# Performance work log

Hardware: AMD Instinct MI355X
Metric: run time of the kernel (lower is better)

Reference implementation:

```python
import jax, jax.numpy as jnp
import numpy as np

WS = 8            # window_size
N = WS * WS       # tokens per window = 64
C = 512           # dim
TEMB = 512        # temb_dim
H = 8             # num_heads
D = C // H        # head_dim = 64
B = 2048          # number of windows (batch * windows per image)


def _rel_pos_index(ws: int) -> np.ndarray:
    coords = np.stack(np.meshgrid(np.arange(ws), np.arange(ws), indexing='ij'))  # (2, ws, ws)
    flat = coords.reshape(2, -1)                      # (2, N)
    rel = flat[:, :, None] - flat[:, None, :]         # (2, N, N)
    rel = rel.transpose(1, 2, 0).copy()               # (N, N, 2)
    rel[:, :, 0] += ws - 1
    rel[:, :, 1] += ws - 1
    rel[:, :, 0] *= 2 * ws - 1
    return rel.sum(-1)                                # (N, N) int

_RP_INDEX = jnp.asarray(_rel_pos_index(WS))           # (N, N)


def setup_inputs() -> dict:
    key = jax.random.key(0)
    ks = jax.random.split(key, 8)
    std = 0.02
    return {
        'x': jax.random.normal(ks[0], (B, N, C), dtype=jnp.float32),
        'temb': jax.random.normal(ks[1], (B, TEMB), dtype=jnp.float32),
        'w_qkv': jax.random.normal(ks[2], (C, 3 * C), dtype=jnp.float32) * std,
        'b_qkv': jnp.zeros((3 * C,), dtype=jnp.float32),
        'w_qkv_t': jax.random.normal(ks[3], (TEMB, 3 * C), dtype=jnp.float32) * std,
        'w_proj': jax.random.normal(ks[4], (C, C), dtype=jnp.float32) * std,
        'b_proj': jnp.zeros((C,), dtype=jnp.float32),
        'rpb_table': jax.random.normal(ks[5], ((2 * WS - 1) ** 2, H), dtype=jnp.float32) * std,
    }


def reference(x, temb, w_qkv, b_qkv, w_qkv_t, w_proj, b_proj, rpb_table):
    # x: (B, N, C), temb: (B, TEMB)
    scale = D ** (-0.5)
    qkv = x @ w_qkv + b_qkv + (temb @ w_qkv_t)[:, None, :]     # (B, N, 3C)
    qkv = qkv.reshape(x.shape[0], N, 3, H, D)
    q = qkv[:, :, 0].transpose(0, 2, 1, 3)                      # (B, H, N, D)
    k = qkv[:, :, 1].transpose(0, 2, 1, 3)
    v = qkv[:, :, 2].transpose(0, 2, 1, 3)
    attn = jnp.einsum('bhnd,bhmd->bhnm', q * scale, k)          # (B, H, N, N)
    bias = rpb_table[_RP_INDEX]                                 # (N, N, H)
    attn = attn + bias.transpose(2, 0, 1)[None]                 # + (1, H, N, N)
    attn = jax.nn.softmax(attn, axis=-1)
    out = jnp.einsum('bhnm,bhmd->bhnd', attn, v)                # (B, H, N, D)
    out = out.transpose(0, 2, 1, 3).reshape(x.shape[0], N, C)   # (B, N, C)
    return out @ w_proj + b_proj
```

## Files before the change

kernel.cpp:

```cpp
#include <hip/hip_runtime.h>

typedef __bf16 bf16;
typedef __bf16 bf16x4 __attribute__((ext_vector_type(4)));
typedef __bf16 bf16x8 __attribute__((ext_vector_type(8)));
typedef float f32x4 __attribute__((ext_vector_type(4)));

#define MFMA(a, b, c) __builtin_amdgcn_mfma_f32_16x16x32_bf16((a), (b), (c), 0, 0, 0)

constexpr size_t SEC = (size_t)2048 * 8 * 64 * 64;

template <bool B> struct BC { static constexpr bool v = B; };

__device__ __forceinline__ void gload16(const void* g, void* l) {
  __builtin_amdgcn_global_load_lds((const __attribute__((address_space(1))) void*)g,
                                   (__attribute__((address_space(3))) void*)l, 16, 0, 0);
}

__global__ void transpose_cast(const float* __restrict__ in, bf16* __restrict__ out,
                               int R, int C) {
  int i = blockIdx.x * 256 + threadIdx.x;
  if (i >= R * C) return;
  int r = i / C, c = i - r * C;
  out[(size_t)c * R + r] = (bf16)in[i];
}

__global__ __launch_bounds__(256) void gemm_temb(
    const float* __restrict__ Ap, const bf16* __restrict__ Bt,
    const float* __restrict__ bias, float* __restrict__ C,
    int M, int N, int K) {
  __shared__ bf16 lA[128 * 32];
  __shared__ bf16 lB[128 * 32];
  const int t = threadIdx.x, l = t & 63;
  const int w = t >> 6, wr = w >> 1, wc = w & 1;
  const int li = l & 15, kl = (l >> 4) << 3;
  const long bm0 = (long)blockIdx.x * 128, bn0 = (long)blockIdx.y * 128;
  f32x4 acc[4][4] = {};
  for (int ks = 0; ks < (K >> 5); ++ks) {
    const int k0 = ks << 5;
    __syncthreads();
#pragma unroll
    for (int i = 0; i < 2; ++i) {
      int u = t + (i << 8);
      int row = u >> 2, kc = (u & 3) << 3;
      const float* ag = Ap + (bm0 + row) * K + k0 + kc;
      f32x4 v0 = *((const f32x4*)ag);
      f32x4 v1 = *((const f32x4*)(ag + 4));
      bf16x8 pk;
      pk[0] = (bf16)v0[0]; pk[1] = (bf16)v0[1]; pk[2] = (bf16)v0[2]; pk[3] = (bf16)v0[3];
      pk[4] = (bf16)v1[0]; pk[5] = (bf16)v1[1]; pk[6] = (bf16)v1[2]; pk[7] = (bf16)v1[3];
      *((bf16x8*)&lA[u << 3]) = pk;
      *((bf16x8*)&lB[u << 3]) = *((const bf16x8*)&Bt[(bn0 + row) * K + k0 + kc]);
    }
    __syncthreads();
    bf16x8 af[4], bfr[4];
#pragma unroll
    for (int mt = 0; mt < 4; ++mt)
      af[mt] = *((const bf16x8*)&lA[(wr * 64 + mt * 16 + li) * 32 + kl]);
#pragma unroll
    for (int nt = 0; nt < 4; ++nt)
      bfr[nt] = *((const bf16x8*)&lB[(wc * 64 + nt * 16 + li) * 32 + kl]);
#pragma unroll
    for (int mt = 0; mt < 4; ++mt)
#pragma unroll
      for (int nt = 0; nt < 4; ++nt)
        acc[mt][nt] = MFMA(af[mt], bfr[nt], acc[mt][nt]);
  }
#pragma unroll
  for (int mt = 0; mt < 4; ++mt)
#pragma unroll
    for (int nt = 0; nt < 4; ++nt) {
      long col = bn0 + wc * 64 + nt * 16 + li;
      float bv = bias[col];
#pragma unroll
      for (int r = 0; r < 4; ++r) {
        long row = bm0 + wr * 64 + mt * 16 + ((l >> 4) << 2) + r;
        C[row * N + col] = acc[mt][nt][r] + bv;
      }
    }
}

template <int MODE>
__global__ __launch_bounds__(256) void mm128(
    const void* __restrict__ Ap, const bf16* __restrict__ Bt,
    const float* __restrict__ biasv, void* __restrict__ Cp) {
  __shared__ bf16 lA[128 * 32];
  __shared__ bf16 lB[128 * 32];
  const int t = threadIdx.x, l = t & 63;
  const int w = t >> 6, wr = w >> 1, wc = w & 1;
  const int li = l & 15, lg = l >> 4;
  const int bm0 = blockIdx.y * 128;
  const int bnG = blockIdx.x * 128;
  const bool isv = (MODE == 1) && (bnG >= 1024);
  const int arow = t >> 1, acol = (t & 1) << 4;

  f32x4 acc[4][4] = {};

  auto kloop = [&](auto swc) {
    constexpr bool SW = decltype(swc)::v;
    f32x4 pf[4];
    if (MODE == 1) {
      const float* xg = (const float*)Ap + (size_t)(bm0 + arow) * 512 + acol;
#pragma unroll
      for (int j = 0; j < 4; ++j) pf[j] = *((const f32x4*)(xg + 4 * j));
    }
    for (int ks = 0; ks < 16; ++ks) {
      const int k0 = ks << 5;
      __syncthreads();
      if (MODE == 1) {
#pragma unroll
        for (int j = 0; j < 2; ++j) {
          bf16x8 pk;
#pragma unroll
          for (int e = 0; e < 4; ++e) {
            pk[e] = (bf16)pf[2 * j][e];
            pk[e + 4] = (bf16)pf[2 * j + 1][e];
          }
          int s = (acol >> 3) + j;
          int p = s ^ ((arow >> 1) & 3);
          *((bf16x8*)&lA[arow * 32 + p * 8]) = pk;
        }
      } else {
#pragma unroll
        for (int i = 0; i < 2; ++i) {
          int u = t + (i << 8);
          int row = u >> 2, p = u & 3;
          int c0 = k0 + ((p ^ ((row >> 1) & 3)) << 3);
          int gr = bm0 + row;
          const bf16* src = (const bf16*)Ap +
                            (((size_t)(gr >> 6) * 8 + (c0 >> 6)) << 12) +
                            (gr & 63) * 64 + (c0 & 63);
          gload16(src, &lA[(w * 64 + (i << 8)) * 8]);
        }
      }
#pragma unroll
      for (int i = 0; i < 2; ++i) {
        int u = t + (i << 8);
        int row = u >> 2, p = u & 3;
        int c0 = k0 + ((p ^ ((row >> 1) & 3)) << 3);
        gload16(Bt + (size_t)(bnG + row) * 512 + c0, &lB[(w * 64 + (i << 8)) * 8]);
      }
      __syncthreads();
      if (MODE == 1 && ks < 15) {
        const float* xg = (const float*)Ap + (size_t)(bm0 + arow) * 512 + k0 + 32 + acol;
#pragma unroll
        for (int j = 0; j < 4; ++j) pf[j] = *((const f32x4*)(xg + 4 * j));
      }
      bf16x8 af[4], bfr[4];
#pragma unroll
      for (int mt = 0; mt < 4; ++mt) {
        int row = wr * 64 + mt * 16 + li;
        af[mt] = *((const bf16x8*)&lA[row * 32 + ((lg ^ ((row >> 1) & 3)) << 3)]);
      }
#pragma unroll
      for (int nt = 0; nt < 4; ++nt) {
        int row = wc * 64 + nt * 16 + li;
        bfr[nt] = *((const bf16x8*)&lB[row * 32 + ((lg ^ ((row >> 1) & 3)) << 3)]);
      }
#pragma unroll
      for (int mt = 0; mt < 4; ++mt)
#pragma unroll
        for (int nt = 0; nt < 4; ++nt)
          acc[mt][nt] = SW ? MFMA(bfr[nt], af[mt], acc[mt][nt])
                           : MFMA(af[mt], bfr[nt], acc[mt][nt]);
    }
  };
  if (isv) kloop(BC<true>{}); else kloop(BC<false>{});

  if (MODE == 0) {
    float* C = (float*)Cp;
#pragma unroll
    for (int nt = 0; nt < 4; ++nt) {
      int col = bnG + wc * 64 + nt * 16 + li;
      float bv = biasv[col];
#pragma unroll
      for (int mt = 0; mt < 4; ++mt) {
        int row = bm0 + wr * 64 + mt * 16 + (lg << 2);
#pragma unroll
        for (int r = 0; r < 4; ++r)
          C[(size_t)(row + r) * 512 + col] = acc[mt][nt][r] + bv;
      }
    }
  } else if (!isv) {
    bf16* qkv = (bf16*)Cp;
    const int b = (bm0 >> 6) + wr;
#pragma unroll
    for (int nt = 0; nt < 4; ++nt) {
      int col = bnG + wc * 64 + nt * 16 + li;
      int sec = col >> 9, h = (col >> 6) & 7, d = col & 63;
      float bv = biasv[(size_t)b * 1536 + col];
      float sc = (sec == 0) ? 0.125f : 1.0f;
      bf16* dst = qkv + (size_t)sec * SEC + (((size_t)b * 8 + h) << 12) + d;
#pragma unroll
      for (int mt = 0; mt < 4; ++mt) {
        int n0 = mt * 16 + (lg << 2);
#pragma unroll
        for (int r = 0; r < 4; ++r)
          dst[(n0 + r) * 64] = (bf16)((acc[mt][nt][r] + bv) * sc);
      }
    }
  } else {
    bf16* qkv = (bf16*)Cp;
    const int b = (bm0 >> 6) + wr;
#pragma unroll
    for (int nt = 0; nt < 4; ++nt) {
      int colb = bnG + wc * 64 + nt * 16 + (lg << 2);
#pragma unroll
      for (int r = 0; r < 4; ++r) {
        int col = colb + r;
        int h = (col >> 6) & 7, d = col & 63;
        float bv = biasv[(size_t)b * 1536 + col];
        bf16* dst = qkv + 2 * SEC + (((size_t)b * 8 + h) << 12) + d * 64;
#pragma unroll
        for (int mt = 0; mt < 4; ++mt) {
          int n = mt * 16 + li;
          dst[n] = (bf16)(acc[mt][nt][r] + bv);
        }
      }
    }
  }
}

__global__ __launch_bounds__(256, 4) void attn_win(bf16* qkv,
                                                   const float* __restrict__ rpb) {
  __shared__ bf16 stg[2][3][4096];
  const int b = blockIdx.x, t = threadIdx.x, l = t & 63, w = t >> 6;
  const int li = l & 15, lg = l >> 4;

  int rpidx[4][4];
#pragma unroll
  for (int ct = 0; ct < 4; ++ct)
#pragma unroll
    for (int r = 0; r < 4; ++r) {
      int n = 16 * w + (lg << 2) + r, m = 16 * ct + li;
      rpidx[ct][r] = (((n >> 3) - (m >> 3) + 7) * 15 + ((n & 7) - (m & 7) + 7)) * 8;
    }

  auto stage = [&](int h, int buf) {
#pragma unroll
    for (int tt = 0; tt < 3; ++tt) {
      const bf16* src = qkv + (size_t)tt * SEC + (((size_t)b * 8 + h) << 12);
#pragma unroll
      for (int i = 0; i < 2; ++i) {
        int u = t + (i << 8);
        int row = u >> 3, s = u & 7;
        gload16(src + row * 64 + ((s ^ (row & 7)) << 3),
                &stg[buf][tt][(w * 64 + (i << 8)) * 8]);
      }
    }
  };

  stage(0, 0);
  for (int h = 0; h < 8; ++h) {
    const int buf = h & 1;
    __syncthreads();
    if (h < 7) stage(h + 1, buf ^ 1);
    bf16* Q = stg[buf][0];
    const bf16* K = stg[buf][1];
    const bf16* V = stg[buf][2];

    f32x4 accS[4] = {};
#pragma unroll
    for (int kk = 0; kk < 2; ++kk) {
      int row = 16 * w + li;
      bf16x8 aq = *((const bf16x8*)&Q[row * 64 + (((kk * 4 + lg) ^ (row & 7)) << 3)]);
#pragma unroll
      for (int ct = 0; ct < 4; ++ct) {
        int kr = 16 * ct + li;
        bf16x8 bk = *((const bf16x8*)&K[kr * 64 + (((kk * 4 + lg) ^ (kr & 7)) << 3)]);
        accS[ct] = MFMA(aq, bk, accS[ct]);
      }
    }
    const float* rpbh = rpb + h;
    float sv[4][4], rsum[4];
#pragma unroll
    for (int ct = 0; ct < 4; ++ct)
#pragma unroll
      for (int r = 0; r < 4; ++r)
        sv[ct][r] = accS[ct][r] + rpbh[rpidx[ct][r]];
#pragma unroll
    for (int r = 0; r < 4; ++r) {
      float m = fmaxf(fmaxf(sv[0][r], sv[1][r]), fmaxf(sv[2][r], sv[3][r]));
      m = fmaxf(m, __shfl_xor(m, 1));
      m = fmaxf(m, __shfl_xor(m, 2));
      m = fmaxf(m, __shfl_xor(m, 4));
      m = fmaxf(m, __shfl_xor(m, 8));
      float s = 0.f;
#pragma unroll
      for (int ct = 0; ct < 4; ++ct) {
        float p = __expf(sv[ct][r] - m);
        sv[ct][r] = p;
        s += p;
      }
      s += __shfl_xor(s, 1);
      s += __shfl_xor(s, 2);
      s += __shfl_xor(s, 4);
      s += __shfl_xor(s, 8);
      rsum[r] = s;
    }
#pragma unroll
    for (int ct = 0; ct < 4; ++ct)
#pragma unroll
      for (int r = 0; r < 4; ++r) {
        int row = 16 * w + (lg << 2) + r;
        int col = 16 * ct + li;
        Q[row * 64 + (((col >> 3) ^ (row & 7)) << 3) + (col & 7)] = (bf16)sv[ct][r];
      }
    f32x4 accO[4] = {};
#pragma unroll
    for (int kk = 0; kk < 2; ++kk) {
      int row = 16 * w + li;
      bf16x8 ap = *((const bf16x8*)&Q[row * 64 + (((kk * 4 + lg) ^ (row & 7)) << 3)]);
#pragma unroll
      for (int ct = 0; ct < 4; ++ct) {
        int vr = 16 * ct + li;
        bf16x8 bv = *((const bf16x8*)&V[vr * 64 + (((kk * 4 + lg) ^ (vr & 7)) << 3)]);
        accO[ct] = MFMA(ap, bv, accO[ct]);
      }
    }
    bf16* ob = qkv + (((size_t)b * 8 + h) << 12);
    float rinv[4];
#pragma unroll
    for (int r = 0; r < 4; ++r) rinv[r] = 1.0f / rsum[r];
#pragma unroll
    for (int ct = 0; ct < 4; ++ct)
#pragma unroll
      for (int r = 0; r < 4; ++r)
        ob[(16 * w + (lg << 2) + r) * 64 + 16 * ct + li] = (bf16)(accO[ct][r] * rinv[r]);
  }
}

extern "C" void kernel_launch(void* const* d_in, const int* in_sizes, int n_in,
                              void* d_out, int out_size, void* d_ws, size_t ws_size,
                              hipStream_t stream) {
  (void)in_sizes; (void)n_in; (void)out_size; (void)ws_size;
  const float* x       = (const float*)d_in[0];
  const float* temb    = (const float*)d_in[1];
  const float* w_qkv   = (const float*)d_in[2];
  const float* b_qkv   = (const float*)d_in[3];
  const float* w_qkv_t = (const float*)d_in[4];
  const float* w_proj  = (const float*)d_in[5];
  const float* b_proj  = (const float*)d_in[6];
  const float* rpb     = (const float*)d_in[7];
  float* out = (float*)d_out;

  char* ws = (char*)d_ws;
  size_t off = 0;
  auto take = [&](size_t bytes) {
    void* p = ws + off;
    off += (bytes + 255) & ~(size_t)255;
    return p;
  };
  bf16* w1t  = (bf16*)take((size_t)1536 * 512 * 2);
  bf16* w3t  = (bf16*)take((size_t)1536 * 512 * 2);
  bf16* w2t  = (bf16*)take((size_t)512 * 512 * 2);
  float* tb  = (float*)take((size_t)2048 * 1536 * 4);
  bf16* qkv  = (bf16*)take(3 * SEC * 2);

  transpose_cast<<<(512 * 1536 + 255) / 256, 256, 0, stream>>>(w_qkv, w1t, 512, 1536);
  transpose_cast<<<(512 * 1536 + 255) / 256, 256, 0, stream>>>(w_qkv_t, w3t, 512, 1536);
  transpose_cast<<<(512 * 512 + 255) / 256, 256, 0, stream>>>(w_proj, w2t, 512, 512);

  gemm_temb<<<dim3(2048 / 128, 1536 / 128), 256, 0, stream>>>(
      temb, w3t, b_qkv, tb, 2048, 1536, 512);

  mm128<1><<<dim3(12, 1024), 256, 0, stream>>>(x, w1t, tb, qkv);

  attn_win<<<2048, 256, 0, stream>>>(qkv, rpb);

  mm128<0><<<dim3(4, 1024), 256, 0, stream>>>(qkv, w2t, b_proj, out);
}
```

Baseline: 915.1 us.

## Double-buffer GEMM LDS staging, pre-cast x to bf16, remap blocks per XCD

The GEMM kernel now double-buffers its LDS tiles and issues async global-to-LDS loads for the next k-step while the current one runs MFMAs, leaving one barrier per iteration. The fp32 input x is cast to bf16 in a separate pass so the QKV GEMM can use the same direct LDS loads instead of in-register conversion. The grid is flattened and remapped so consecutive blocks on each XCD share M rows, aiming for better L2 reuse. This costs an extra full read and write of x and doubles LDS use per block, which may lower occupancy.

```diff
diff --git a/kernel.cpp b/kernel.cpp
--- a/kernel.cpp
+++ b/kernel.cpp
@@ -22,6 +22,17 @@
   if (i >= R * C) return;
   int r = i / C, c = i - r * C;
   out[(size_t)c * R + r] = (bf16)in[i];
+}
+
+__global__ __launch_bounds__(256) void cast_bf16(const float* __restrict__ in,
+                                                 bf16* __restrict__ out) {
+  size_t i = ((size_t)blockIdx.x * 256 + threadIdx.x) * 8;
+  f32x4 v0 = *((const f32x4*)(in + i));
+  f32x4 v1 = *((const f32x4*)(in + i + 4));
+  bf16x8 pk;
+  pk[0] = (bf16)v0[0]; pk[1] = (bf16)v0[1]; pk[2] = (bf16)v0[2]; pk[3] = (bf16)v0[3];
+  pk[4] = (bf16)v1[0]; pk[5] = (bf16)v1[1]; pk[6] = (bf16)v1[2]; pk[7] = (bf16)v1[3];
+  *((bf16x8*)(out + i)) = pk;
 }
 
 __global__ __launch_bounds__(256) void gemm_temb(
@@ -83,78 +94,60 @@
 __global__ __launch_bounds__(256) void mm128(
     const void* __restrict__ Ap, const bf16* __restrict__ Bt,
     const float* __restrict__ biasv, void* __restrict__ Cp) {
-  __shared__ bf16 lA[128 * 32];
-  __shared__ bf16 lB[128 * 32];
+  __shared__ bf16 lA[2][128 * 32];
+  __shared__ bf16 lB[2][128 * 32];
+  constexpr int NB = (MODE == 1) ? 12 : 4;
   const int t = threadIdx.x, l = t & 63;
   const int w = t >> 6, wr = w >> 1, wc = w & 1;
   const int li = l & 15, lg = l >> 4;
-  const int bm0 = blockIdx.y * 128;
-  const int bnG = blockIdx.x * 128;
+
+  const int wg = blockIdx.x;
+  const int xcd = wg & 7, idx = wg >> 3;
+  const int mb = xcd * 128 + idx / NB;
+  const int nb = idx % NB;
+  const int bm0 = mb * 128, bnG = nb * 128;
   const bool isv = (MODE == 1) && (bnG >= 1024);
-  const int arow = t >> 1, acol = (t & 1) << 4;
+
+  const int srow = t >> 2, sp = t & 3;
+
+  auto stage = [&](int ks, int buf) {
+    const int k0 = ks << 5;
+#pragma unroll
+    for (int i = 0; i < 2; ++i) {
+      int row = srow + (i << 6);
+      int c0 = k0 + ((sp ^ ((row >> 1) & 3)) << 3);
+      const bf16* asrc;
+      if (MODE == 1) {
+        asrc = (const bf16*)Ap + (size_t)(bm0 + row) * 512 + c0;
+      } else {
+        int gr = bm0 + row;
+        asrc = (const bf16*)Ap + (((size_t)(gr >> 6) * 8 + (c0 >> 6)) << 12) +
+               (gr & 63) * 64 + (c0 & 63);
+      }
+      gload16(asrc, &lA[buf][(w * 64 + (i << 8)) * 8]);
+      gload16(Bt + (size_t)(bnG + row) * 512 + c0, &lB[buf][(w * 64 + (i << 8)) * 8]);
+    }
+  };
 
   f32x4 acc[4][4] = {};
 
   auto kloop = [&](auto swc) {
     constexpr bool SW = decltype(swc)::v;
-    f32x4 pf[4];
-    if (MODE == 1) {
-      const float* xg = (const float*)Ap + (size_t)(bm0 + arow) * 512 + acol;
-#pragma unroll
-      for (int j = 0; j < 4; ++j) pf[j] = *((const f32x4*)(xg + 4 * j));
-    }
+    stage(0, 0);
+    __syncthreads();
+    int cb = 0;
     for (int ks = 0; ks < 16; ++ks) {
-      const int k0 = ks << 5;
-      __syncthreads();
-      if (MODE == 1) {
-#pragma unroll
-        for (int j = 0; j < 2; ++j) {
-          bf16x8 pk;
-#pragma unroll
-          for (int e = 0; e < 4; ++e) {
-            pk[e] = (bf16)pf[2 * j][e];
-            pk[e + 4] = (bf16)pf[2 * j + 1][e];
-          }
-          int s = (acol >> 3) + j;
-          int p = s ^ ((arow >> 1) & 3);
-          *((bf16x8*)&lA[arow * 32 + p * 8]) = pk;
-        }
-      } else {
-#pragma unroll
-        for (int i = 0; i < 2; ++i) {
-          int u = t + (i << 8);
-          int row = u >> 2, p = u & 3;
-          int c0 = k0 + ((p ^ ((row >> 1) & 3)) << 3);
-          int gr = bm0 + row;
-          const bf16* src = (const bf16*)Ap +
-                            (((size_t)(gr >> 6) * 8 + (c0 >> 6)) << 12) +
-                            (gr & 63) * 64 + (c0 & 63);
-          gload16(src, &lA[(w * 64 + (i << 8)) * 8]);
-        }
-      }
-#pragma unroll
-      for (int i = 0; i < 2; ++i) {
-        int u = t + (i << 8);
-        int row = u >> 2, p = u & 3;
-        int c0 = k0 + ((p ^ ((row >> 1) & 3)) << 3);
-        gload16(Bt + (size_t)(bnG + row) * 512 + c0, &lB[(w * 64 + (i << 8)) * 8]);
-      }
-      __syncthreads();
-      if (MODE == 1 && ks < 15) {
-        const float* xg = (const float*)Ap + (size_t)(bm0 + arow) * 512 + k0 + 32 + acol;
-#pragma unroll
-        for (int j = 0; j < 4; ++j) pf[j] = *((const f32x4*)(xg + 4 * j));
-      }
+      if (ks < 15) stage(ks + 1, cb ^ 1);
       bf16x8 af[4], bfr[4];
 #pragma unroll
       for (int mt = 0; mt < 4; ++mt) {
         int row = wr * 64 + mt * 16 + li;
-        af[mt] = *((const bf16x8*)&lA[row * 32 + ((lg ^ ((row >> 1) & 3)) << 3)]);
+        af[mt] = *((const bf16x8*)&lA[cb][row * 32 + ((lg ^ ((row >> 1) & 3)) << 3)]);
       }
 #pragma unroll
       for (int nt = 0; nt < 4; ++nt) {
         int row = wc * 64 + nt * 16 + li;
-        bfr[nt] = *((const bf16x8*)&lB[row * 32 + ((lg ^ ((row >> 1) & 3)) << 3)]);
+        bfr[nt] = *((const bf16x8*)&lB[cb][row * 32 + ((lg ^ ((row >> 1) & 3)) << 3)]);
       }
 #pragma unroll
       for (int mt = 0; mt < 4; ++mt)
@@ -162,6 +155,8 @@
         for (int nt = 0; nt < 4; ++nt)
           acc[mt][nt] = SW ? MFMA(bfr[nt], af[mt], acc[mt][nt])
                            : MFMA(af[mt], bfr[nt], acc[mt][nt]);
+      __syncthreads();
+      cb ^= 1;
     }
   };
   if (isv) kloop(BC<true>{}); else kloop(BC<false>{});
@@ -355,17 +350,20 @@
   bf16* w2t  = (bf16*)take((size_t)512 * 512 * 2);
   float* tb  = (float*)take((size_t)2048 * 1536 * 4);
   bf16* qkv  = (bf16*)take(3 * SEC * 2);
+  bf16* xb   = (bf16*)take((size_t)131072 * 512 * 2);
 
   transpose_cast<<<(512 * 1536 + 255) / 256, 256, 0, stream>>>(w_qkv, w1t, 512, 1536);
   transpose_cast<<<(512 * 1536 + 255) / 256, 256, 0, stream>>>(w_qkv_t, w3t, 512, 1536);
   transpose_cast<<<(512 * 512 + 255) / 256, 256, 0, stream>>>(w_proj, w2t, 512, 512);
 
+  cast_bf16<<<(131072 * 512 / 8) / 256, 256, 0, stream>>>(x, xb);
+
   gemm_temb<<<dim3(2048 / 128, 1536 / 128), 256, 0, stream>>>(
       temb, w3t, b_qkv, tb, 2048, 1536, 512);
 
-  mm128<1><<<dim3(12, 1024), 256, 0, stream>>>(x, w1t, tb, qkv);
+  mm128<1><<<12 * 1024, 256, 0, stream>>>(xb, w1t, tb, qkv);
 
   attn_win<<<2048, 256, 0, stream>>>(qkv, rpb);
 
-  mm128<0><<<dim3(4, 1024), 256, 0, stream>>>(qkv, w2t, b_proj, out);
-}
+  mm128<0><<<4 * 1024, 256, 0, stream>>>(qkv, w2t, b_proj, out);
+}
```

New measurement: 767.2 us. -16.2%, faster.
